# Optimization experiments

Measured on AMD Instinct MI355X. Metric: run time of the kernel, lower is better.

The kernel has to match this reference:

```python
import jax, jax.numpy as jnp
import numpy as np

D_MODEL = 1024
N_HEAD = 16
HEAD_DIM = D_MODEL // N_HEAD
SCALING = HEAD_DIM ** (-0.5)


def setup_inputs() -> dict:
    key0 = jax.random.key(0)
    ks = jax.random.split(key0, 12)
    B, Q, K = 2, 2048, 2048
    bound = 1.0 / np.sqrt(D_MODEL)
    def lin(kw, kb):
        W = jax.random.uniform(kw, (D_MODEL, D_MODEL), jnp.float32, -bound, bound)
        b = jax.random.uniform(kb, (D_MODEL,), jnp.float32, -bound, bound)
        return W, b
    Wq, bq = lin(ks[0], ks[1])
    Wk, bk = lin(ks[2], ks[3])
    Wv, bv = lin(ks[4], ks[5])
    Wo, bo = lin(ks[6], ks[7])
    return {
        "query": jax.random.normal(ks[8], (B, Q, D_MODEL), jnp.float32),
        "key": jax.random.normal(ks[9], (B, K, D_MODEL), jnp.float32),
        "value": jax.random.normal(ks[10], (B, K, D_MODEL), jnp.float32),
        "encoder_attn_mask": jax.random.randint(ks[11], (B, K), 0, 2).astype(bool),
        "Wq": Wq, "bq": bq, "Wk": Wk, "bk": bk,
        "Wv": Wv, "bv": bv, "Wo": Wo, "bo": bo,
    }


def reference(query, key, value, encoder_attn_mask, Wq, bq, Wk, bk, Wv, bv, Wo, bo):
    B, Qlen, _ = query.shape
    Klen = key.shape[1]
    q = (query @ Wq.T + bq) * SCALING
    k = key @ Wk.T + bk
    v = value @ Wv.T + bv
    q = q.reshape(B, Qlen, N_HEAD, HEAD_DIM)
    k = k.reshape(B, Klen, N_HEAD, HEAD_DIM)
    v = v.reshape(B, Klen, N_HEAD, HEAD_DIM)
    # scores: [batch, q, k, heads]
    attn = jnp.einsum('bqnh,bknh->bqkn', q, k)
    mask = encoder_attn_mask[:, None, :, None]  # (B,1,K,1)
    attn = jnp.where(mask, -jnp.inf, attn)
    attn_weights = jax.nn.softmax(attn, axis=2)  # dropout p=0.0
    out = jnp.einsum('bqkn,bknh->bqnh', attn_weights, v).reshape(B, Qlen, D_MODEL)
    out = out @ Wo.T + bo
    return out, attn_weights
```

## Files before the change

### kernel.cpp

```cpp
#include <hip/hip_runtime.h>
#include <hip/hip_fp16.h>

#define B_  2
#define S_  2048
#define NH  16
#define HD  64
#define DM  1024
#define SCAL 0.125f
#define BSN (B_*S_*NH)

typedef _Float16 f16;
typedef _Float16 f16x4 __attribute__((ext_vector_type(4)));
typedef _Float16 f16x8 __attribute__((ext_vector_type(8)));
typedef float    f32x4 __attribute__((ext_vector_type(4)));

#define MFMA16(a,b,c) __builtin_amdgcn_mfma_f32_16x16x32_f16(a,b,c,0,0,0)

template<int MODE>
__global__ __launch_bounds__(256) void gemm_k(const float* __restrict__ X,
    const float* __restrict__ W, const float* __restrict__ bias,
    void* __restrict__ outp, float scale)
{
    __shared__ __align__(16) f16 As[128][40];
    __shared__ __align__(16) f16 Bs[128][40];
    const int tid = threadIdx.x;
    const int wave = tid >> 6, lane = tid & 63;
    const int wm = wave >> 1, wn = wave & 1;
    const int lr = lane & 15, lg = lane >> 4;
    const int m0 = blockIdx.x * 128, n0 = blockIdx.y * 128;

    f32x4 acc[4][4];
    #pragma unroll
    for (int s = 0; s < 4; s++)
        #pragma unroll
        for (int f = 0; f < 4; f++) acc[s][f] = (f32x4)(0.0f);

    const int srow = tid >> 3;
    const int sk4  = (tid & 7) * 4;

    for (int kt = 0; kt < DM; kt += 32) {
        __syncthreads();
        #pragma unroll
        for (int i = 0; i < 4; i++) {
            const int r = srow + i * 32;
            float4 va;
            const float* xp = X + (size_t)(m0 + r) * DM + kt + sk4;
            if (MODE == 3) {
                float4 p0 = *(const float4*)xp;
                float4 p1 = *(const float4*)(xp + 4194304);
                va.x = p0.x + p1.x;
                va.y = p0.y + p1.y;
                va.z = p0.z + p1.z;
                va.w = p0.w + p1.w;
            } else {
                va = *(const float4*)xp;
            }
            f16x4 ha = { (f16)va.x, (f16)va.y, (f16)va.z, (f16)va.w };
            *(f16x4*)&As[r][sk4] = ha;
            float4 vb = *(const float4*)(W + (size_t)(n0 + r) * DM + kt + sk4);
            f16x4 hb = { (f16)vb.x, (f16)vb.y, (f16)vb.z, (f16)vb.w };
            *(f16x4*)&Bs[r][sk4] = hb;
        }
        __syncthreads();
        f16x8 af[4], bf[4];
        #pragma unroll
        for (int s = 0; s < 4; s++) af[s] = *(const f16x8*)&As[wm*64 + s*16 + lr][lg*8];
        #pragma unroll
        for (int f = 0; f < 4; f++) bf[f] = *(const f16x8*)&Bs[wn*64 + f*16 + lr][lg*8];
        #pragma unroll
        for (int s = 0; s < 4; s++)
            #pragma unroll
            for (int f = 0; f < 4; f++)
                acc[s][f] = MFMA16(af[s], bf[f], acc[s][f]);
    }

    float bcol[4];
    #pragma unroll
    for (int f = 0; f < 4; f++) bcol[f] = bias[n0 + wn*64 + f*16 + lr];

    #pragma unroll
    for (int s = 0; s < 4; s++) {
        const int mg = m0 + wm*64 + s*16 + lg*4;
        #pragma unroll
        for (int f = 0; f < 4; f++) {
            const int nc = n0 + wn*64 + f*16 + lr;
            if (MODE == 3) {
                float* o = (float*)outp;
                #pragma unroll
                for (int r = 0; r < 4; r++)
                    o[(size_t)(mg + r) * DM + nc] = acc[s][f][r] + bcol[f];
            } else {
                const int b = mg >> 11, seq = mg & 2047;
                const int head = nc >> 6, h = nc & 63;
                f16* o = (f16*)outp;
                if (MODE == 2) {
                    f16x4 pk = { (f16)(acc[s][f][0] + bcol[f]), (f16)(acc[s][f][1] + bcol[f]),
                                 (f16)(acc[s][f][2] + bcol[f]), (f16)(acc[s][f][3] + bcol[f]) };
                    *(f16x4*)&o[((size_t)((b*NH + head)*HD + h)) * S_ + seq] = pk;
                } else {
                    #pragma unroll
                    for (int r = 0; r < 4; r++)
                        o[((size_t)(b*NH + head) * S_ + seq + r) * HD + h] =
                            (f16)((acc[s][f][r] + bcol[f]) * scale);
                }
            }
        }
    }
}

__global__ __launch_bounds__(256) void sums_k(const f16* __restrict__ qw,
    const f16* __restrict__ kw, const int* __restrict__ amask, float* __restrict__ lpart)
{
    const int tid = threadIdx.x, wave = tid >> 6, lane = tid & 63;
    const int lr = lane & 15, lg = lane >> 4;
    const int qt = blockIdx.x, kc = blockIdx.y, b = blockIdx.z;
    const int q0 = qt * 16, k0b = kc * 512;

    float rs[4][4];
    #pragma unroll
    for (int i = 0; i < 4; i++)
        #pragma unroll
        for (int r = 0; r < 4; r++) rs[i][r] = 0.f;

    f16x8 qf[4][2];
    #pragma unroll
    for (int hh = 0; hh < 4; hh++) {
        const int n = wave * 4 + hh;
        const f16* qp = qw + ((size_t)((b*NH + n) * S_) + q0 + lr) * HD + lg * 8;
        qf[hh][0] = *(const f16x8*)qp;
        qf[hh][1] = *(const f16x8*)(qp + 32);
    }
    for (int kt = 0; kt < 8; kt++) {
        const int k0 = k0b + kt * 64;
        int km[4];
        #pragma unroll
        for (int ct = 0; ct < 4; ct++) km[ct] = amask[b * S_ + k0 + ct*16 + lr];
        #pragma unroll
        for (int hh = 0; hh < 4; hh++) {
            const int n = wave * 4 + hh;
            const f16* kp = kw + ((size_t)((b*NH + n) * S_) + k0) * HD;
            #pragma unroll
            for (int ct = 0; ct < 4; ct++) {
                f16x8 b0 = *(const f16x8*)(kp + (size_t)(ct*16 + lr) * HD + lg*8);
                f16x8 b1 = *(const f16x8*)(kp + (size_t)(ct*16 + lr) * HD + 32 + lg*8);
                f32x4 sv = (f32x4)(0.f);
                sv = MFMA16(qf[hh][0], b0, sv);
                sv = MFMA16(qf[hh][1], b1, sv);
                #pragma unroll
                for (int r = 0; r < 4; r++) rs[hh][r] += km[ct] ? 0.f : __expf(sv[r]);
            }
        }
    }
    #pragma unroll
    for (int hh = 0; hh < 4; hh++) {
        #pragma unroll
        for (int r = 0; r < 4; r++) {
            float v = rs[hh][r];
            v += __shfl_xor(v, 1);  v += __shfl_xor(v, 2);
            v += __shfl_xor(v, 4);  v += __shfl_xor(v, 8);
            if (lr == 0)
                lpart[(size_t)kc * BSN +
                      (size_t)(b*S_ + q0 + lg*4 + r) * NH + wave*4 + hh] = v;
        }
    }
}

__global__ __launch_bounds__(512) void attn_k(const f16* __restrict__ qw,
    const f16* __restrict__ kw, const f16* __restrict__ vt,
    const int* __restrict__ amask, const float* __restrict__ lpart,
    float* __restrict__ attn, float* __restrict__ op)
{
    extern __shared__ float Ps[];
    const int tid = threadIdx.x, wave = tid >> 6, lane = tid & 63;
    const int lr = lane & 15, lg = lane >> 4;
    const int qt = blockIdx.x, kq = blockIdx.y, b = blockIdx.z;
    const int q0 = qt * 16;
    const int k0b = kq * 1024;

    f16x8 qf[2][2];
    float rl[2][4];
    #pragma unroll
    for (int hh = 0; hh < 2; hh++) {
        const int n = wave * 2 + hh;
        const f16* qp = qw + ((size_t)((b*NH + n) * S_) + q0 + lr) * HD + lg * 8;
        qf[hh][0] = *(const f16x8*)qp;
        qf[hh][1] = *(const f16x8*)(qp + 32);
        #pragma unroll
        for (int r = 0; r < 4; r++) {
            const float* lp = lpart + (size_t)(b*S_ + q0 + lg*4 + r) * NH + n;
            rl[hh][r] = 1.0f / (lp[0] + lp[BSN] + lp[2*BSN] + lp[3*BSN]);
        }
    }
    f32x4 accO[2][4];
    #pragma unroll
    for (int i = 0; i < 2; i++)
        #pragma unroll
        for (int j = 0; j < 4; j++) accO[i][j] = (f32x4)(0.f);

    for (int kt = 0; kt < 16; kt++) {
        const int k0 = k0b + kt * 64;
        int km[4];
        #pragma unroll
        for (int ct = 0; ct < 4; ct++) km[ct] = amask[b * S_ + k0 + ct*16 + lr];
        #pragma unroll
        for (int hh = 0; hh < 2; hh++) {
            const int n = wave * 2 + hh;
            const f16* kp = kw + ((size_t)((b*NH + n) * S_) + k0) * HD;
            f32x4 sfr[4];
            #pragma unroll
            for (int ct = 0; ct < 4; ct++) {
                f16x8 b0 = *(const f16x8*)(kp + (size_t)(ct*16 + lr) * HD + lg*8);
                f16x8 b1 = *(const f16x8*)(kp + (size_t)(ct*16 + lr) * HD + 32 + lg*8);
                f32x4 sv = (f32x4)(0.f);
                sv = MFMA16(qf[hh][0], b0, sv);
                sv = MFMA16(qf[hh][1], b1, sv);
                sfr[ct] = sv;
            }
            float* myP = Ps + (size_t)n * (16 * 68);
            #pragma unroll
            for (int ct = 0; ct < 4; ct++) {
                #pragma unroll
                for (int r = 0; r < 4; r++) {
                    float p = km[ct] ? 0.0f : __expf(sfr[ct][r]) * rl[hh][r];
                    myP[(lg*4 + r) * 68 + ct*16 + lr] = p;
                }
            }
            f32x4 pa00 = *(const f32x4*)&myP[lr * 68 + lg*8];
            f32x4 pa01 = *(const f32x4*)&myP[lr * 68 + lg*8 + 4];
            f32x4 pa10 = *(const f32x4*)&myP[lr * 68 + 32 + lg*8];
            f32x4 pa11 = *(const f32x4*)&myP[lr * 68 + 32 + lg*8 + 4];
            f16x8 a0 = { (f16)pa00[0], (f16)pa00[1], (f16)pa00[2], (f16)pa00[3],
                         (f16)pa01[0], (f16)pa01[1], (f16)pa01[2], (f16)pa01[3] };
            f16x8 a1 = { (f16)pa10[0], (f16)pa10[1], (f16)pa10[2], (f16)pa10[3],
                         (f16)pa11[0], (f16)pa11[1], (f16)pa11[2], (f16)pa11[3] };
            #pragma unroll
            for (int hb = 0; hb < 4; hb++) {
                const f16* vp = vt + ((size_t)((b*NH + n) * HD) + hb*16 + lr) * S_ + k0;
                f16x8 v0 = *(const f16x8*)(vp + lg*8);
                f16x8 v1 = *(const f16x8*)(vp + 32 + lg*8);
                accO[hh][hb] = MFMA16(a0, v0, accO[hh][hb]);
                accO[hh][hb] = MFMA16(a1, v1, accO[hh][hb]);
            }
        }
        __syncthreads();
        {
            const int kk = tid & 63;
            #pragma unroll
            for (int it = 0; it < 2; it++) {
                const int q = (tid >> 6) + it * 8;
                float pv[16];
                #pragma unroll
                for (int n = 0; n < 16; n++)
                    pv[n] = Ps[n * (16*68) + q * 68 + kk];
                float* dst = attn + ((size_t)(b*S_ + q0 + q) * S_ + k0 + kk) * NH;
                #pragma unroll
                for (int j = 0; j < 4; j++)
                    *(float4*)(dst + j*4) = make_float4(pv[j*4+0], pv[j*4+1],
                                                        pv[j*4+2], pv[j*4+3]);
            }
        }
        __syncthreads();
    }
    float* opk = op + (size_t)kq * 4194304;
    #pragma unroll
    for (int hh = 0; hh < 2; hh++) {
        const int n = wave * 2 + hh;
        #pragma unroll
        for (int hb = 0; hb < 4; hb++)
            #pragma unroll
            for (int r = 0; r < 4; r++)
                opk[(size_t)(b*S_ + q0 + lg*4 + r) * DM + n*HD + hb*16 + lr] = accO[hh][hb][r];
    }
}

extern "C" void kernel_launch(void* const* d_in, const int* in_sizes, int n_in,
                              void* d_out, int out_size, void* d_ws, size_t ws_size,
                              hipStream_t stream)
{
    const float* query = (const float*)d_in[0];
    const float* key   = (const float*)d_in[1];
    const float* value = (const float*)d_in[2];
    const int*   amask = (const int*)d_in[3];
    const float* Wq = (const float*)d_in[4];
    const float* bq = (const float*)d_in[5];
    const float* Wk = (const float*)d_in[6];
    const float* bk = (const float*)d_in[7];
    const float* Wv = (const float*)d_in[8];
    const float* bv = (const float*)d_in[9];
    const float* Wo = (const float*)d_in[10];
    const float* bo = (const float*)d_in[11];

    char* ws = (char*)d_ws;
    f16*   qw = (f16*)(ws + 0);
    f16*   kw = (f16*)(ws + 8388608);
    f16*   vt = (f16*)(ws + 16777216);
    float* lp = (float*)(ws + 25165824);
    float* op = (float*)(ws + 26214400);

    float* out0 = (float*)d_out;
    float* attn = out0 + 4194304;

    dim3 blk(256);
    dim3 g1(32, 8);
    gemm_k<0><<<g1, blk, 0, stream>>>(query, Wq, bq, (void*)qw, SCAL);
    gemm_k<1><<<g1, blk, 0, stream>>>(key,   Wk, bk, (void*)kw, 1.0f);
    gemm_k<2><<<g1, blk, 0, stream>>>(value, Wv, bv, (void*)vt, 1.0f);
    sums_k<<<dim3(128, 4, 2), blk, 0, stream>>>(qw, kw, amask, lp);
    attn_k<<<dim3(128, 2, 2), dim3(512), 69632, stream>>>(qw, kw, vt, amask, lp, attn, op);
    gemm_k<3><<<g1, blk, 0, stream>>>(op, Wo, bo, d_out, 1.0f);
}
```

Measured before the change: 1.180 ms.

## Double-buffer P tile in attention kernel, overlap attn store with next tile

The attention kernel now works on 32-key tiles and keeps two LDS buffers for the probability tile. Each iteration writes the previous tile's attention weights to global memory with nontemporal stores, which lets one barrier per iteration replace two and overlaps the output writes with the next tile's MFMA work. It also adds a launch-bounds occupancy hint, an odd LDS stride to avoid bank conflicts, and partial unrolling of the sums kernel loop. In exchange there are twice as many loop iterations, each with less MFMA work, and the larger LDS footprint and register cap may limit occupancy or cause spills.

```diff
diff --git a/kernel.cpp b/kernel.cpp
--- a/kernel.cpp
+++ b/kernel.cpp
@@ -130,6 +130,7 @@
         qf[hh][0] = *(const f16x8*)qp;
         qf[hh][1] = *(const f16x8*)(qp + 32);
     }
+    #pragma unroll 2
     for (int kt = 0; kt < 8; kt++) {
         const int k0 = k0b + kt * 64;
         int km[4];
@@ -165,7 +166,10 @@
     }
 }
 
-__global__ __launch_bounds__(512) void attn_k(const f16* __restrict__ qw,
+#define PSTR 35
+#define PBUF (16*16*PSTR)
+
+__global__ __launch_bounds__(512, 4) void attn_k(const f16* __restrict__ qw,
     const f16* __restrict__ kw, const f16* __restrict__ vt,
     const int* __restrict__ amask, const float* __restrict__ lpart,
     float* __restrict__ attn, float* __restrict__ op)
@@ -176,6 +180,8 @@
     const int qt = blockIdx.x, kq = blockIdx.y, b = blockIdx.z;
     const int q0 = qt * 16;
     const int k0b = kq * 1024;
+    const int wq = tid >> 5;
+    const int wk = tid & 31;
 
     f16x8 qf[2][2];
     float rl[2][4];
@@ -197,18 +203,34 @@
         #pragma unroll
         for (int j = 0; j < 4; j++) accO[i][j] = (f32x4)(0.f);
 
-    for (int kt = 0; kt < 16; kt++) {
-        const int k0 = k0b + kt * 64;
-        int km[4];
-        #pragma unroll
-        for (int ct = 0; ct < 4; ct++) km[ct] = amask[b * S_ + k0 + ct*16 + lr];
+    for (int t = 0; t < 32; t++) {
+        const int k0 = k0b + t * 32;
+        float* Pb = Ps + (t & 1) * PBUF;
+
+        if (t > 0) {
+            const float* Pp = Ps + ((t - 1) & 1) * PBUF;
+            float pv[16];
+            #pragma unroll
+            for (int n = 0; n < 16; n++)
+                pv[n] = Pp[n * (16*PSTR) + wq * PSTR + wk];
+            float* dst = attn + ((size_t)(b*S_ + q0 + wq) * S_ + (k0 - 32) + wk) * NH;
+            #pragma unroll
+            for (int j = 0; j < 4; j++) {
+                f32x4 sv = { pv[j*4+0], pv[j*4+1], pv[j*4+2], pv[j*4+3] };
+                __builtin_nontemporal_store(sv, (f32x4*)(dst + j*4));
+            }
+        }
+
+        int km[2];
+        #pragma unroll
+        for (int ct = 0; ct < 2; ct++) km[ct] = amask[b * S_ + k0 + ct*16 + lr];
         #pragma unroll
         for (int hh = 0; hh < 2; hh++) {
             const int n = wave * 2 + hh;
             const f16* kp = kw + ((size_t)((b*NH + n) * S_) + k0) * HD;
-            f32x4 sfr[4];
-            #pragma unroll
-            for (int ct = 0; ct < 4; ct++) {
+            f32x4 sfr[2];
+            #pragma unroll
+            for (int ct = 0; ct < 2; ct++) {
                 f16x8 b0 = *(const f16x8*)(kp + (size_t)(ct*16 + lr) * HD + lg*8);
                 f16x8 b1 = *(const f16x8*)(kp + (size_t)(ct*16 + lr) * HD + 32 + lg*8);
                 f32x4 sv = (f32x4)(0.f);
@@ -216,51 +238,48 @@
                 sv = MFMA16(qf[hh][1], b1, sv);
                 sfr[ct] = sv;
             }
-            float* myP = Ps + (size_t)n * (16 * 68);
-            #pragma unroll
-            for (int ct = 0; ct < 4; ct++) {
+            float* myP = Pb + n * (16*PSTR);
+            #pragma unroll
+            for (int ct = 0; ct < 2; ct++) {
                 #pragma unroll
                 for (int r = 0; r < 4; r++) {
                     float p = km[ct] ? 0.0f : __expf(sfr[ct][r]) * rl[hh][r];
-                    myP[(lg*4 + r) * 68 + ct*16 + lr] = p;
+                    myP[(lg*4 + r) * PSTR + ct*16 + lr] = p;
                 }
             }
-            f32x4 pa00 = *(const f32x4*)&myP[lr * 68 + lg*8];
-            f32x4 pa01 = *(const f32x4*)&myP[lr * 68 + lg*8 + 4];
-            f32x4 pa10 = *(const f32x4*)&myP[lr * 68 + 32 + lg*8];
-            f32x4 pa11 = *(const f32x4*)&myP[lr * 68 + 32 + lg*8 + 4];
-            f16x8 a0 = { (f16)pa00[0], (f16)pa00[1], (f16)pa00[2], (f16)pa00[3],
-                         (f16)pa01[0], (f16)pa01[1], (f16)pa01[2], (f16)pa01[3] };
-            f16x8 a1 = { (f16)pa10[0], (f16)pa10[1], (f16)pa10[2], (f16)pa10[3],
-                         (f16)pa11[0], (f16)pa11[1], (f16)pa11[2], (f16)pa11[3] };
+            f32x4 pa0 = *(const f32x4*)&myP[lr * PSTR + lg*8];
+            f32x4 pa1 = *(const f32x4*)&myP[lr * PSTR + lg*8 + 4];
+            f16x8 a0 = { (f16)pa0[0], (f16)pa0[1], (f16)pa0[2], (f16)pa0[3],
+                         (f16)pa1[0], (f16)pa1[1], (f16)pa1[2], (f16)pa1[3] };
             #pragma unroll
             for (int hb = 0; hb < 4; hb++) {
                 const f16* vp = vt + ((size_t)((b*NH + n) * HD) + hb*16 + lr) * S_ + k0;
                 f16x8 v0 = *(const f16x8*)(vp + lg*8);
-                f16x8 v1 = *(const f16x8*)(vp + 32 + lg*8);
                 accO[hh][hb] = MFMA16(a0, v0, accO[hh][hb]);
-                accO[hh][hb] = MFMA16(a1, v1, accO[hh][hb]);
-            }
-        }
-        __syncthreads();
-        {
-            const int kk = tid & 63;
-            #pragma unroll
-            for (int it = 0; it < 2; it++) {
-                const int q = (tid >> 6) + it * 8;
-                float pv[16];
-                #pragma unroll
-                for (int n = 0; n < 16; n++)
-                    pv[n] = Ps[n * (16*68) + q * 68 + kk];
-                float* dst = attn + ((size_t)(b*S_ + q0 + q) * S_ + k0 + kk) * NH;
-                #pragma unroll
-                for (int j = 0; j < 4; j++)
-                    *(float4*)(dst + j*4) = make_float4(pv[j*4+0], pv[j*4+1],
-                                                        pv[j*4+2], pv[j*4+3]);
-            }
-        }
-        __syncthreads();
-    }
+            }
+        }
+
+        __builtin_amdgcn_sched_barrier(0);
+        asm volatile("s_waitcnt lgkmcnt(0)" ::: "memory");
+        __builtin_amdgcn_s_barrier();
+        __builtin_amdgcn_sched_barrier(0);
+    }
+
+    {
+        const float* Pp = Ps + PBUF;
+        const int k0 = k0b + 31 * 32;
+        float pv[16];
+        #pragma unroll
+        for (int n = 0; n < 16; n++)
+            pv[n] = Pp[n * (16*PSTR) + wq * PSTR + wk];
+        float* dst = attn + ((size_t)(b*S_ + q0 + wq) * S_ + k0 + wk) * NH;
+        #pragma unroll
+        for (int j = 0; j < 4; j++) {
+            f32x4 sv = { pv[j*4+0], pv[j*4+1], pv[j*4+2], pv[j*4+3] };
+            __builtin_nontemporal_store(sv, (f32x4*)(dst + j*4));
+        }
+    }
+
     float* opk = op + (size_t)kq * 4194304;
     #pragma unroll
     for (int hh = 0; hh < 2; hh++) {
@@ -306,6 +325,6 @@
     gemm_k<1><<<g1, blk, 0, stream>>>(key,   Wk, bk, (void*)kw, 1.0f);
     gemm_k<2><<<g1, blk, 0, stream>>>(value, Wv, bv, (void*)vt, 1.0f);
     sums_k<<<dim3(128, 4, 2), blk, 0, stream>>>(qw, kw, amask, lp);
-    attn_k<<<dim3(128, 2, 2), dim3(512), 69632, stream>>>(qw, kw, vt, amask, lp, attn, op);
+    attn_k<<<dim3(128, 2, 2), dim3(512), 71680, stream>>>(qw, kw, vt, amask, lp, attn, op);
     gemm_k<3><<<g1, blk, 0, stream>>>(op, Wo, bo, d_out, 1.0f);
 }
```

After: 1.546 ms. 31.0% more time.
